# Kernel tuning notes

Measured on AMD Instinct MI355X. Metric: run time of the kernel, lower is better.

Reference implementation:

```python
import jax, jax.numpy as jnp
import numpy as np

B, T, H = 128, 2048, 512

def setup_inputs() -> dict:
    key = jax.random.key(0)
    k1, k2, k3, k4, k5 = jax.random.split(key, 5)
    scale = 1.0 / np.sqrt(H)
    return {
        "query": jax.random.normal(k1, (B, H), dtype=jnp.float32),
        "key": jax.random.normal(k2, (B, T, H), dtype=jnp.float32),
        "w1": jax.random.normal(k3, (H, H), dtype=jnp.float32) * scale,
        "w2": jax.random.normal(k4, (H, H), dtype=jnp.float32) * scale,
        "w_out": jax.random.normal(k5, (H,), dtype=jnp.float32) * scale,
    }

def reference(query, key, w1, w2, w_out):
    # attn_weight = w_out . tanh(relu(W1 q) + relu(W2 k)), softmax over T, weighted sum of key
    q_h = jax.nn.relu(jnp.einsum('bh,gh->bg', query, w1))            # (B, H)
    k_h = jax.nn.relu(jnp.einsum('bth,gh->btg', key, w2))            # (B, T, H)
    scores = jnp.einsum('btg,g->bt', jnp.tanh(q_h[:, None, :] + k_h), w_out)  # (B, T)
    attn = jax.nn.softmax(scores, axis=1)                            # (B, T)
    return jnp.einsum('bt,bth->bh', attn, key)                       # (B, H)
```

## Files before the change

### kernel.cpp

```cpp
#include <hip/hip_runtime.h>
#include <hip/hip_bf16.h>

#define B_N 128
#define T_N 2048
#define H_N 512

typedef __attribute__((ext_vector_type(8))) short bf16x8;
typedef __attribute__((ext_vector_type(4))) float f32x4;

union U4 { unsigned int i[4]; bf16x8 v; };

__device__ __forceinline__ unsigned int f2bf(float f) {
    unsigned int u = __float_as_uint(f);
    u += 0x7fffu + ((u >> 16) & 1u);
    return u >> 16;
}

__device__ __forceinline__ unsigned int cvtpk(float lo, float hi) {
    unsigned int r;
    asm("v_cvt_pk_bf16_f32 %0, %1, %2" : "=v"(r) : "v"(lo), "v"(hi));
    return r;
}

__device__ __forceinline__ float tanh_fast(float x) {
    float e = __expf(2.f * x);
    float r = __builtin_amdgcn_rcpf(e + 1.f);
    return 1.f - 2.f * r;
}

#define FENCE asm volatile("" ::: "memory")
#define SBAR  do { FENCE; __builtin_amdgcn_s_barrier(); FENCE; } while (0)
#define VMCNT(n) asm volatile("s_waitcnt vmcnt(" #n ")" ::: "memory")
#define LGKM0    asm volatile("s_waitcnt lgkmcnt(0)" ::: "memory")
#define SCHED0   __builtin_amdgcn_sched_barrier(0)

__global__ void k_w2prep(const float* __restrict__ w2, unsigned short* __restrict__ w2p) {
    int t = blockIdx.x * 256 + threadIdx.x;
    int l  = t & 63;
    int n  = (t >> 6) & 3;
    int ks = (t >> 8) & 15;
    int wc = t >> 12;
    int g  = wc * 64 + n * 16 + (l & 15);
    int k0 = ks * 32 + (l >> 4) * 8;
    const float4* s = reinterpret_cast<const float4*>(w2 + (size_t)g * H_N + k0);
    float4 f0 = s[0], f1 = s[1];
    uint4 p;
    p.x = f2bf(f0.x) | (f2bf(f0.y) << 16);
    p.y = f2bf(f0.z) | (f2bf(f0.w) << 16);
    p.z = f2bf(f1.x) | (f2bf(f1.y) << 16);
    p.w = f2bf(f1.z) | (f2bf(f1.w) << 16);
    *reinterpret_cast<uint4*>(reinterpret_cast<char*>(w2p) + (size_t)t * 16) = p;
}

__global__ void k_qh(const float* __restrict__ query, const float* __restrict__ w1,
                     float* __restrict__ qh) {
    int b = blockIdx.x;
    int g = threadIdx.x;
    __shared__ float q[H_N];
    q[g] = query[(size_t)b * H_N + g];
    __syncthreads();
    const float4* w = reinterpret_cast<const float4*>(w1 + (size_t)g * H_N);
    float acc = 0.f;
#pragma unroll 4
    for (int i = 0; i < H_N / 4; ++i) {
        float4 wv = w[i];
        acc += q[4*i] * wv.x + q[4*i+1] * wv.y + q[4*i+2] * wv.z + q[4*i+3] * wv.w;
    }
    qh[(size_t)b * H_N + g] = fmaxf(acc, 0.f);
}

__global__ __launch_bounds__(512, 4) void k_scores(
    const float* __restrict__ key, const unsigned short* __restrict__ w2p,
    const float* __restrict__ qh, const float* __restrict__ w_out,
    float* __restrict__ partial, float* __restrict__ psum)
{
    const int b    = blockIdx.y;
    const int chnk = blockIdx.x;
    const int t0   = chnk * 64;
    const int tid  = threadIdx.x;
    const int wid  = tid >> 6;
    const int lane = tid & 63;
    const int lrow = lane & 15;
    const int lq   = lane >> 4;
    const int xm   = lrow & 7;

    __shared__ __align__(16) char Ab[65536];
    __shared__ float sscore[8][64];
    __shared__ float wlds[64];

    const int arow = tid >> 3;
    const int acol = tid & 7;
    const int axm  = arow & 7;
    const float* asrc = key + ((size_t)b * T_N + t0 + arow) * H_N + acol * 16;

    const char* bptr = reinterpret_cast<const char*>(w2p) + wid * 65536 + lane * 16;

    float4 Ra[4], Rb[4];
    bf16x8 br0[4], br1[4];

#define ALOAD(p, R) do {                                                      \
        const float4* q_ = reinterpret_cast<const float4*>(asrc + (p) * 128); \
        R[0] = q_[0]; R[1] = q_[1]; R[2] = q_[2]; R[3] = q_[3];               \
    } while (0)

#define AWRITE(p, R) do {                                                     \
        U4 u0_, u1_;                                                          \
        u0_.i[0] = cvtpk(R[0].x, R[0].y); u0_.i[1] = cvtpk(R[0].z, R[0].w);   \
        u0_.i[2] = cvtpk(R[1].x, R[1].y); u0_.i[3] = cvtpk(R[1].z, R[1].w);   \
        u1_.i[0] = cvtpk(R[2].x, R[2].y); u1_.i[1] = cvtpk(R[2].z, R[2].w);   \
        u1_.i[2] = cvtpk(R[3].x, R[3].y); u1_.i[3] = cvtpk(R[3].z, R[3].w);   \
        *reinterpret_cast<bf16x8*>(Ab + arow * 1024 +                         \
            ((((p) * 16 + acol * 2)     ^ axm) << 4)) = u0_.v;                \
        *reinterpret_cast<bf16x8*>(Ab + arow * 1024 +                         \
            ((((p) * 16 + acol * 2 + 1) ^ axm) << 4)) = u1_.v;                \
    } while (0)

#define LOADB(sl, R) do {                                                     \
        R[0] = *reinterpret_cast<const bf16x8*>(bptr + (sl) * 4096);          \
        R[1] = *reinterpret_cast<const bf16x8*>(bptr + (sl) * 4096 + 1024);   \
        R[2] = *reinterpret_cast<const bf16x8*>(bptr + (sl) * 4096 + 2048);   \
        R[3] = *reinterpret_cast<const bf16x8*>(bptr + (sl) * 4096 + 3072);   \
    } while (0)

    f32x4 acc[4][4];

#define KSTEP(ks, CUR, CNT, ISSUE) do {                                       \
        bf16x8 av_[4];                                                        \
        _Pragma("unroll")                                                     \
        for (int m_ = 0; m_ < 4; ++m_)                                        \
            av_[m_] = *reinterpret_cast<const bf16x8*>(                       \
                Ab + (m_ * 16 + lrow) * 1024 + ((((ks) * 4 + lq) ^ xm) << 4));\
        VMCNT(CNT);                                                           \
        SCHED0;                                                               \
        __builtin_amdgcn_s_setprio(1);                                        \
        _Pragma("unroll")                                                     \
        for (int m_ = 0; m_ < 4; ++m_) {                                      \
            acc[m_][0] = __builtin_amdgcn_mfma_f32_16x16x32_bf16(av_[m_], CUR[0], acc[m_][0], 0, 0, 0); \
            acc[m_][1] = __builtin_amdgcn_mfma_f32_16x16x32_bf16(av_[m_], CUR[1], acc[m_][1], 0, 0, 0); \
            acc[m_][2] = __builtin_amdgcn_mfma_f32_16x16x32_bf16(av_[m_], CUR[2], acc[m_][2], 0, 0, 0); \
            acc[m_][3] = __builtin_amdgcn_mfma_f32_16x16x32_bf16(av_[m_], CUR[3], acc[m_][3], 0, 0, 0); \
        }                                                                     \
        __builtin_amdgcn_s_setprio(0);                                        \
        if (ISSUE) LOADB((ks) + 2, CUR);                                      \
    } while (0)

    ALOAD(0, Ra); ALOAD(1, Rb);
    VMCNT(4);  AWRITE(0, Ra); ALOAD(2, Ra);
    VMCNT(4);  AWRITE(1, Rb); ALOAD(3, Rb);
    VMCNT(4);  AWRITE(2, Ra);
    LOADB(0, br0); LOADB(1, br1);
    VMCNT(8);  AWRITE(3, Rb);
    LGKM0;
    SBAR;

#pragma unroll
    for (int m = 0; m < 4; ++m)
#pragma unroll
        for (int n = 0; n < 4; ++n) acc[m][n] = f32x4{0.f, 0.f, 0.f, 0.f};

    KSTEP(0,  br0, 4, 1); KSTEP(1,  br1, 4, 1);
    KSTEP(2,  br0, 4, 1); KSTEP(3,  br1, 4, 1);
    KSTEP(4,  br0, 4, 1); KSTEP(5,  br1, 4, 1);
    KSTEP(6,  br0, 4, 1); KSTEP(7,  br1, 4, 1);
    KSTEP(8,  br0, 4, 1); KSTEP(9,  br1, 4, 1);
    KSTEP(10, br0, 4, 1); KSTEP(11, br1, 4, 1);
    KSTEP(12, br0, 4, 1); KSTEP(13, br1, 4, 1);
    KSTEP(14, br0, 4, 0); KSTEP(15, br1, 0, 0);

    float pscore[4][4] = {};
#pragma unroll
    for (int n = 0; n < 4; ++n) {
        int g = wid * 64 + n * 16 + lrow;
        float wo = w_out[g];
        float qv = qh[(size_t)b * H_N + g];
#pragma unroll
        for (int m = 0; m < 4; ++m)
#pragma unroll
            for (int r = 0; r < 4; ++r) {
                float x = qv + fmaxf(acc[m][n][r], 0.f);
                pscore[m][r] = fmaf(wo, tanh_fast(x), pscore[m][r]);
            }
    }

#pragma unroll
    for (int m = 0; m < 4; ++m)
#pragma unroll
        for (int r = 0; r < 4; ++r) {
            float v = pscore[m][r];
            v += __shfl_xor(v, 1);
            v += __shfl_xor(v, 2);
            v += __shfl_xor(v, 4);
            v += __shfl_xor(v, 8);
            if (lrow == 0) sscore[wid][m * 16 + lq * 4 + r] = v;
        }
    __syncthreads();

    if (tid < 64) {
        float s = 0.f;
#pragma unroll
        for (int w = 0; w < 8; ++w) s += sscore[w][tid];
        wlds[tid] = __expf(s);
    }
    __syncthreads();

    if (wid == 0) {
        float v = wlds[lane];
        v += __shfl_xor(v, 1);
        v += __shfl_xor(v, 2);
        v += __shfl_xor(v, 4);
        v += __shfl_xor(v, 8);
        v += __shfl_xor(v, 16);
        v += __shfl_xor(v, 32);
        if (lane == 0) psum[b * 32 + chnk] = v;
    }

    float pv[8] = {};
#pragma unroll
    for (int i = 0; i < 8; ++i) {
        int t = wid * 8 + i;
        bf16x8 kv = *reinterpret_cast<const bf16x8*>(
            Ab + t * 1024 + ((lane ^ i) << 4));
        float wt = wlds[t];
#pragma unroll
        for (int e = 0; e < 8; ++e)
            pv[e] = fmaf(wt, __uint_as_float((unsigned)(unsigned short)kv[e] << 16), pv[e]);
    }
    __syncthreads();

    float* pvred = reinterpret_cast<float*>(Ab);
    {
        float4 lo, hi;
        lo.x = pv[0]; lo.y = pv[1]; lo.z = pv[2]; lo.w = pv[3];
        hi.x = pv[4]; hi.y = pv[5]; hi.z = pv[6]; hi.w = pv[7];
        *reinterpret_cast<float4*>(pvred + wid * 512 + lane * 8)     = lo;
        *reinterpret_cast<float4*>(pvred + wid * 512 + lane * 8 + 4) = hi;
    }
    __syncthreads();
    {
        float s = 0.f;
#pragma unroll
        for (int w = 0; w < 8; ++w) s += pvred[w * 512 + tid];
        partial[((size_t)(b * 32 + chnk)) * H_N + tid] = s;
    }

#undef ALOAD
#undef AWRITE
#undef LOADB
#undef KSTEP
}

__global__ void k_out(const float* __restrict__ partial, const float* __restrict__ psum,
                      float* __restrict__ out) {
    int idx = blockIdx.x * 256 + threadIdx.x;
    int b = idx >> 9, h = idx & 511;
    float s = 0.f, d = 0.f;
#pragma unroll
    for (int c = 0; c < 32; ++c) {
        s += partial[((size_t)(b * 32 + c)) * H_N + h];
        d += psum[b * 32 + c];
    }
    out[idx] = s / d;
}

extern "C" void kernel_launch(void* const* d_in, const int* in_sizes, int n_in,
                              void* d_out, int out_size, void* d_ws, size_t ws_size,
                              hipStream_t stream) {
    const float* query = (const float*)d_in[0];
    const float* key   = (const float*)d_in[1];
    const float* w1    = (const float*)d_in[2];
    const float* w2    = (const float*)d_in[3];
    const float* w_out = (const float*)d_in[4];
    float* out = (float*)d_out;

    char* ws = (char*)d_ws;
    unsigned short* w2p = (unsigned short*)(ws);
    float* qh      = (float*)(ws + 524288);
    float* partial = (float*)(ws + 1048576);
    float* psum    = (float*)(ws + 9437184);

    hipLaunchKernelGGL(k_w2prep, dim3(128),     dim3(256), 0, stream, w2, w2p);
    hipLaunchKernelGGL(k_qh,     dim3(128),     dim3(512), 0, stream, query, w1, qh);
    hipLaunchKernelGGL(k_scores, dim3(32, 128), dim3(512), 0, stream,
                       key, w2p, qh, w_out, partial, psum);
    hipLaunchKernelGGL(k_out,    dim3(256),     dim3(256), 0, stream, partial, psum, out);
}
```

Before: 239.5 us.

## Process two 64-row tiles per scores block and prefetch the next tile

Each k_scores block now handles two consecutive 64-token chunks, and the grid is halved. Global loads for the second key tile are issued during the epilogue of the first tile (tanh, softmax partials and weighted sum), so memory latency overlaps compute and there are fewer block launches. The cost is a longer serial block, fewer blocks to fill the GPU (2048 instead of 4096), extra register pressure from the prefetch buffers, and hand-tuned vmcnt waits that must match the number of outstanding loads.

```diff
diff --git a/kernel.cpp b/kernel.cpp
--- a/kernel.cpp
+++ b/kernel.cpp
@@ -76,7 +76,6 @@
 {
     const int b    = blockIdx.y;
     const int chnk = blockIdx.x;
-    const int t0   = chnk * 64;
     const int tid  = threadIdx.x;
     const int wid  = tid >> 6;
     const int lane = tid & 63;
@@ -91,15 +90,15 @@
     const int arow = tid >> 3;
     const int acol = tid & 7;
     const int axm  = arow & 7;
-    const float* asrc = key + ((size_t)b * T_N + t0 + arow) * H_N + acol * 16;
+    const float* asrc0 = key + ((size_t)b * T_N + chnk * 128 + arow) * H_N + acol * 16;
 
     const char* bptr = reinterpret_cast<const char*>(w2p) + wid * 65536 + lane * 16;
 
     float4 Ra[4], Rb[4];
     bf16x8 br0[4], br1[4];
 
-#define ALOAD(p, R) do {                                                      \
-        const float4* q_ = reinterpret_cast<const float4*>(asrc + (p) * 128); \
+#define ALOAD(BASE, p, R) do {                                                \
+        const float4* q_ = reinterpret_cast<const float4*>((BASE) + (p) * 128); \
         R[0] = q_[0]; R[1] = q_[1]; R[2] = q_[2]; R[3] = q_[3];               \
     } while (0)
 
@@ -144,9 +143,9 @@
         if (ISSUE) LOADB((ks) + 2, CUR);                                      \
     } while (0)
 
-    ALOAD(0, Ra); ALOAD(1, Rb);
-    VMCNT(4);  AWRITE(0, Ra); ALOAD(2, Ra);
-    VMCNT(4);  AWRITE(1, Rb); ALOAD(3, Rb);
+    ALOAD(asrc0, 0, Ra); ALOAD(asrc0, 1, Rb);
+    VMCNT(4);  AWRITE(0, Ra); ALOAD(asrc0, 2, Ra);
+    VMCNT(4);  AWRITE(1, Rb); ALOAD(asrc0, 3, Rb);
     VMCNT(4);  AWRITE(2, Ra);
     LOADB(0, br0); LOADB(1, br1);
     VMCNT(8);  AWRITE(3, Rb);
@@ -154,93 +153,116 @@
     SBAR;
 
 #pragma unroll
-    for (int m = 0; m < 4; ++m)
-#pragma unroll
-        for (int n = 0; n < 4; ++n) acc[m][n] = f32x4{0.f, 0.f, 0.f, 0.f};
-
-    KSTEP(0,  br0, 4, 1); KSTEP(1,  br1, 4, 1);
-    KSTEP(2,  br0, 4, 1); KSTEP(3,  br1, 4, 1);
-    KSTEP(4,  br0, 4, 1); KSTEP(5,  br1, 4, 1);
-    KSTEP(6,  br0, 4, 1); KSTEP(7,  br1, 4, 1);
-    KSTEP(8,  br0, 4, 1); KSTEP(9,  br1, 4, 1);
-    KSTEP(10, br0, 4, 1); KSTEP(11, br1, 4, 1);
-    KSTEP(12, br0, 4, 1); KSTEP(13, br1, 4, 1);
-    KSTEP(14, br0, 4, 0); KSTEP(15, br1, 0, 0);
-
-    float pscore[4][4] = {};
-#pragma unroll
-    for (int n = 0; n < 4; ++n) {
-        int g = wid * 64 + n * 16 + lrow;
-        float wo = w_out[g];
-        float qv = qh[(size_t)b * H_N + g];
+    for (int jj = 0; jj < 2; ++jj) {
+        const int c32 = chnk * 2 + jj;
+        const float* asrcN = asrc0 + 64 * H_N;
+
 #pragma unroll
         for (int m = 0; m < 4; ++m)
 #pragma unroll
+            for (int n = 0; n < 4; ++n) acc[m][n] = f32x4{0.f, 0.f, 0.f, 0.f};
+
+        KSTEP(0,  br0, 4, 1); KSTEP(1,  br1, 4, 1);
+        KSTEP(2,  br0, 4, 1); KSTEP(3,  br1, 4, 1);
+        KSTEP(4,  br0, 4, 1); KSTEP(5,  br1, 4, 1);
+        KSTEP(6,  br0, 4, 1); KSTEP(7,  br1, 4, 1);
+        KSTEP(8,  br0, 4, 1); KSTEP(9,  br1, 4, 1);
+        KSTEP(10, br0, 4, 1); KSTEP(11, br1, 4, 1);
+        KSTEP(12, br0, 4, 1); KSTEP(13, br1, 4, 1);
+        KSTEP(14, br0, 4, 0); KSTEP(15, br1, 0, 0);
+
+        float pscore[4][4] = {};
+#pragma unroll
+        for (int n = 0; n < 4; ++n) {
+            int g = wid * 64 + n * 16 + lrow;
+            float wo = w_out[g];
+            float qv = qh[(size_t)b * H_N + g];
+#pragma unroll
+            for (int m = 0; m < 4; ++m)
+#pragma unroll
+                for (int r = 0; r < 4; ++r) {
+                    float x = qv + fmaxf(acc[m][n][r], 0.f);
+                    pscore[m][r] = fmaf(wo, tanh_fast(x), pscore[m][r]);
+                }
+        }
+
+        if (jj == 0) { ALOAD(asrcN, 0, Ra); ALOAD(asrcN, 1, Rb); }
+
+#pragma unroll
+        for (int m = 0; m < 4; ++m)
+#pragma unroll
             for (int r = 0; r < 4; ++r) {
-                float x = qv + fmaxf(acc[m][n][r], 0.f);
-                pscore[m][r] = fmaf(wo, tanh_fast(x), pscore[m][r]);
+                float v = pscore[m][r];
+                v += __shfl_xor(v, 1);
+                v += __shfl_xor(v, 2);
+                v += __shfl_xor(v, 4);
+                v += __shfl_xor(v, 8);
+                if (lrow == 0) sscore[wid][m * 16 + lq * 4 + r] = v;
             }
-    }
-
-#pragma unroll
-    for (int m = 0; m < 4; ++m)
-#pragma unroll
-        for (int r = 0; r < 4; ++r) {
-            float v = pscore[m][r];
+        LGKM0; SBAR;
+
+        if (tid < 64) {
+            float s = 0.f;
+#pragma unroll
+            for (int w = 0; w < 8; ++w) s += sscore[w][tid];
+            wlds[tid] = __expf(s);
+        }
+        LGKM0; SBAR;
+
+        if (wid == 0) {
+            float v = wlds[lane];
             v += __shfl_xor(v, 1);
             v += __shfl_xor(v, 2);
             v += __shfl_xor(v, 4);
             v += __shfl_xor(v, 8);
-            if (lrow == 0) sscore[wid][m * 16 + lq * 4 + r] = v;
-        }
-    __syncthreads();
-
-    if (tid < 64) {
-        float s = 0.f;
-#pragma unroll
-        for (int w = 0; w < 8; ++w) s += sscore[w][tid];
-        wlds[tid] = __expf(s);
-    }
-    __syncthreads();
-
-    if (wid == 0) {
-        float v = wlds[lane];
-        v += __shfl_xor(v, 1);
-        v += __shfl_xor(v, 2);
-        v += __shfl_xor(v, 4);
-        v += __shfl_xor(v, 8);
-        v += __shfl_xor(v, 16);
-        v += __shfl_xor(v, 32);
-        if (lane == 0) psum[b * 32 + chnk] = v;
-    }
-
-    float pv[8] = {};
-#pragma unroll
-    for (int i = 0; i < 8; ++i) {
-        int t = wid * 8 + i;
-        bf16x8 kv = *reinterpret_cast<const bf16x8*>(
-            Ab + t * 1024 + ((lane ^ i) << 4));
-        float wt = wlds[t];
-#pragma unroll
-        for (int e = 0; e < 8; ++e)
-            pv[e] = fmaf(wt, __uint_as_float((unsigned)(unsigned short)kv[e] << 16), pv[e]);
-    }
-    __syncthreads();
-
-    float* pvred = reinterpret_cast<float*>(Ab);
-    {
-        float4 lo, hi;
-        lo.x = pv[0]; lo.y = pv[1]; lo.z = pv[2]; lo.w = pv[3];
-        hi.x = pv[4]; hi.y = pv[5]; hi.z = pv[6]; hi.w = pv[7];
-        *reinterpret_cast<float4*>(pvred + wid * 512 + lane * 8)     = lo;
-        *reinterpret_cast<float4*>(pvred + wid * 512 + lane * 8 + 4) = hi;
-    }
-    __syncthreads();
-    {
-        float s = 0.f;
-#pragma unroll
-        for (int w = 0; w < 8; ++w) s += pvred[w * 512 + tid];
-        partial[((size_t)(b * 32 + chnk)) * H_N + tid] = s;
+            v += __shfl_xor(v, 16);
+            v += __shfl_xor(v, 32);
+            if (lane == 0) psum[b * 32 + c32] = v;
+        }
+
+        float pv[8] = {};
+#pragma unroll
+        for (int i = 0; i < 8; ++i) {
+            int t = wid * 8 + i;
+            bf16x8 kv = *reinterpret_cast<const bf16x8*>(
+                Ab + t * 1024 + ((lane ^ i) << 4));
+            float wt = wlds[t];
+#pragma unroll
+            for (int e = 0; e < 8; ++e)
+                pv[e] = fmaf(wt, __uint_as_float((unsigned)(unsigned short)kv[e] << 16), pv[e]);
+        }
+        LGKM0; SBAR;
+
+        float* pvred = reinterpret_cast<float*>(Ab);
+        {
+            float4 lo, hi;
+            lo.x = pv[0]; lo.y = pv[1]; lo.z = pv[2]; lo.w = pv[3];
+            hi.x = pv[4]; hi.y = pv[5]; hi.z = pv[6]; hi.w = pv[7];
+            *reinterpret_cast<float4*>(pvred + wid * 512 + lane * 8)     = lo;
+            *reinterpret_cast<float4*>(pvred + wid * 512 + lane * 8 + 4) = hi;
+        }
+        LGKM0; SBAR;
+        {
+            float s = 0.f;
+#pragma unroll
+            for (int w = 0; w < 8; ++w) s += pvred[w * 512 + tid];
+            partial[((size_t)(b * 32 + c32)) * H_N + tid] = s;
+        }
+
+        if (jj == 0) {
+            LGKM0; SBAR;
+            VMCNT(5);
+            AWRITE(0, Ra); ALOAD(asrcN, 2, Ra);
+            VMCNT(5);
+            AWRITE(1, Rb); ALOAD(asrcN, 3, Rb);
+            LOADB(0, br0); LOADB(1, br1);
+            VMCNT(12);
+            AWRITE(2, Ra);
+            VMCNT(8);
+            AWRITE(3, Rb);
+            LGKM0;
+            SBAR;
+        }
     }
 
 #undef ALOAD
@@ -280,7 +302,7 @@
 
     hipLaunchKernelGGL(k_w2prep, dim3(128),     dim3(256), 0, stream, w2, w2p);
     hipLaunchKernelGGL(k_qh,     dim3(128),     dim3(512), 0, stream, query, w1, qh);
-    hipLaunchKernelGGL(k_scores, dim3(32, 128), dim3(512), 0, stream,
+    hipLaunchKernelGGL(k_scores, dim3(16, 128), dim3(512), 0, stream,
                        key, w2p, qh, w_out, partial, psum);
     hipLaunchKernelGGL(k_out,    dim3(256),     dim3(256), 0, stream, partial, psum, out);
 }
```

Measured after the change: 566.3 us. 2.36x slower.
